# Kernel optimization log

Measured on AMD Instinct MI355X. Metric: run time of the kernel, lower is better.

## Reference

```python
import jax, jax.numpy as jnp
import numpy as np

N = 50000      # nodes per graph side
E = 800000     # edges per graph side
G = 128        # number of graphs in the batch
D = 256        # input feature dim
L = 1024       # number of output labels
NEG_SLOPE = 0.2


def _gat_layer(x, src, dst, W, a_src, a_dst, b, n_nodes):
    """Single-head GATConv with self-loops already included in (src, dst)."""
    h = x @ W                                   # [N, F]
    s_src = h @ a_src                           # [N] per-node source score
    s_dst = h @ a_dst                           # [N] per-node dest score
    e = jax.nn.leaky_relu(s_src[src] + s_dst[dst], NEG_SLOPE)   # [E']
    m = jax.ops.segment_max(e, dst, num_segments=n_nodes)        # segment softmax (stable)
    ex = jnp.exp(e - m[dst])
    denom = jax.ops.segment_sum(ex, dst, num_segments=n_nodes)
    alpha = ex / denom[dst]                     # [E']
    out = jax.ops.segment_sum(h[src] * alpha[:, None], dst, num_segments=n_nodes)
    return out + b


def _mean_pool(x, batch, n_graphs):
    s = jax.ops.segment_sum(x, batch, num_segments=n_graphs)
    cnt = jax.ops.segment_sum(jnp.ones((x.shape[0],), x.dtype), batch, num_segments=n_graphs)
    return s / jnp.maximum(cnt, 1.0)[:, None]


def setup_inputs() -> dict:
    key = jax.random.key(0)
    ks = jax.random.split(key, 24)
    p = lambda k, shape: (jax.random.normal(k, shape, jnp.float32) * 0.05)
    inp = {
        "x_s": jax.random.normal(ks[0], (N, D), jnp.float32),
        "x_t": jax.random.normal(ks[1], (N, D), jnp.float32),
        "edge_index_s": jax.random.randint(ks[2], (2, E), 0, N, jnp.int32),
        "edge_index_t": jax.random.randint(ks[3], (2, E), 0, N, jnp.int32),
        "xs_batch": jnp.sort(jax.random.randint(ks[4], (N,), 0, G, jnp.int32)),
        "xt_batch": jnp.sort(jax.random.randint(ks[5], (N,), 0, G, jnp.int32)),
        # source-graph GAT layers: 256->128, 128->64
        "Ws1": p(ks[6], (D, D // 2)), "as1_src": p(ks[7], (D // 2,)), "as1_dst": p(ks[8], (D // 2,)), "bs1": jnp.zeros((D // 2,), jnp.float32),
        "Ws2": p(ks[9], (D // 2, D // 4)), "as2_src": p(ks[10], (D // 4,)), "as2_dst": p(ks[11], (D // 4,)), "bs2": jnp.zeros((D // 4,), jnp.float32),
        # target-graph GAT layers
        "Wt1": p(ks[12], (D, D // 2)), "at1_src": p(ks[13], (D // 2,)), "at1_dst": p(ks[14], (D // 2,)), "bt1": jnp.zeros((D // 2,), jnp.float32),
        "Wt2": p(ks[15], (D // 2, D // 4)), "at2_src": p(ks[16], (D // 4,)), "at2_dst": p(ks[17], (D // 4,)), "bt2": jnp.zeros((D // 4,), jnp.float32),
        # classifier head
        "Wlin": p(ks[18], (D // 4, L)), "blin": jnp.zeros((L,), jnp.float32),
    }
    return inp


def reference(x_s, x_t, edge_index_s, edge_index_t, xs_batch, xt_batch,
              Ws1, as1_src, as1_dst, bs1, Ws2, as2_src, as2_dst, bs2,
              Wt1, at1_src, at1_dst, bt1, Wt2, at2_src, at2_dst, bt2,
              Wlin, blin):
    loop = jnp.arange(N, dtype=edge_index_s.dtype)
    src_s = jnp.concatenate([edge_index_s[0], loop])   # add self-loops (PyG default)
    dst_s = jnp.concatenate([edge_index_s[1], loop])
    src_t = jnp.concatenate([edge_index_t[0], loop])
    dst_t = jnp.concatenate([edge_index_t[1], loop])

    x1 = jax.nn.relu(_gat_layer(x_s, src_s, dst_s, Ws1, as1_src, as1_dst, bs1, N))
    x2 = jax.nn.relu(_gat_layer(x1, src_s, dst_s, Ws2, as2_src, as2_dst, bs2, N))
    xs = _mean_pool(x2, xs_batch, G)                   # [G, 64]

    x3 = jax.nn.relu(_gat_layer(x_t, src_t, dst_t, Wt1, at1_src, at1_dst, bt1, N))
    x4 = jax.nn.relu(_gat_layer(x3, src_t, dst_t, Wt2, at2_src, at2_dst, bt2, N))
    xt = _mean_pool(x4, xt_batch, G)                   # [G, 64]

    out = (xs + xt) @ Wlin + blin                      # [G, L]
    return jax.nn.sigmoid(out)
```

## Files before the change

### kernel.cpp

```cpp
#include <hip/hip_runtime.h>
#include <hip/hip_bf16.h>
#include <math.h>

constexpr int Nn   = 50000;
constexpr int Ecnt = 800000;
constexpr int Gn   = 128;
constexpr int Din  = 256;
constexpr int Lout = 1024;

constexpr int BKT_SH = 7;
constexpr int NBKT   = (Nn + 127) >> BKT_SH;
constexpr int CHUNK  = 4096;
constexpr int EBC    = (Ecnt + CHUNK - 1) / CHUNK;
constexpr size_t HS  = (size_t)Nn * 64;

typedef __attribute__((ext_vector_type(8))) short short8;
typedef __attribute__((ext_vector_type(4))) float f32x4;
typedef __attribute__((ext_vector_type(2))) float v2f;

__device__ __forceinline__ float lrelu(float x) { return x >= 0.f ? x : 0.2f * x; }

__device__ __forceinline__ float bflo(uint32_t v) { return __uint_as_float(v << 16); }
__device__ __forceinline__ float bfhi(uint32_t v) { return __uint_as_float(v & 0xffff0000u); }
__device__ __forceinline__ uint32_t f2bf(float f) {
    uint32_t x = __float_as_uint(f);
    return (x + 0x7fffu + ((x >> 16) & 1u)) >> 16;
}
__device__ __forceinline__ uint32_t packbf(float lo, float hi) {
    return f2bf(lo) | (f2bf(hi) << 16);
}

__global__ __launch_bounds__(512) void bkt_scan2(const int* __restrict__ bkt_cnt_b,
                                                 int* __restrict__ bkt_ptr_b,
                                                 int* __restrict__ bkt_cur_b,
                                                 int* __restrict__ row_ptr_b) {
    int side = blockIdx.x;
    const int* bkt_cnt = bkt_cnt_b + (size_t)side * (NBKT + 1);
    int* bkt_ptr = bkt_ptr_b + (size_t)side * (NBKT + 1);
    int* bkt_cur = bkt_cur_b + (size_t)side * (NBKT + 1);
    int* row_ptr = row_ptr_b + (size_t)side * (Nn + 1);
    __shared__ int buf[512];
    int t = threadIdx.x;
    int v = (t < NBKT) ? bkt_cnt[t] : 0;
    buf[t] = v;
    __syncthreads();
    for (int off = 1; off < 512; off <<= 1) {
        int x = (t >= off) ? buf[t - off] : 0;
        __syncthreads();
        buf[t] += x;
        __syncthreads();
    }
    if (t < NBKT) {
        int excl = buf[t] - v;
        bkt_ptr[t] = excl;
        bkt_cur[t] = excl;
    }
    if (t == 511) {
        bkt_ptr[NBKT] = buf[511];
        row_ptr[Nn]   = buf[511];
    }
}

__global__ __launch_bounds__(256) void bkt_scatter2(const int* __restrict__ e0,
                                                    const int* __restrict__ e1,
                                                    int* __restrict__ bkt_cur_b,
                                                    uint32_t* __restrict__ bkt_edges_b, int E) {
    int side = blockIdx.y;
    const int* src = side ? e1 : e0;
    const int* dst = src + E;
    int* bkt_cur = bkt_cur_b + (size_t)side * (NBKT + 1);
    uint32_t* bkt_edges = bkt_edges_b + (size_t)side * Ecnt;
    __shared__ int h[NBKT];
    __shared__ int cur[NBKT];
    for (int i = threadIdx.x; i < NBKT; i += 256) h[i] = 0;
    __syncthreads();
    int base = blockIdx.x * CHUNK;
    int end = min(base + CHUNK, E);
    for (int i = base + threadIdx.x; i < end; i += 256)
        atomicAdd(&h[dst[i] >> BKT_SH], 1);
    __syncthreads();
    for (int i = threadIdx.x; i < NBKT; i += 256) {
        int c = h[i];
        h[i] = c ? atomicAdd(&bkt_cur[i], c) : 0;
        cur[i] = 0;
    }
    __syncthreads();
    for (int i = base + threadIdx.x; i < end; i += 256) {
        int d = dst[i], b = d >> BKT_SH;
        int pos = h[b] + atomicAdd(&cur[b], 1);
        bkt_edges[pos] = (uint32_t)src[i] | ((uint32_t)(d & 127) << 16);
    }
}

__global__ __launch_bounds__(256) void csr_finalize2(const uint32_t* __restrict__ bkt_edges_b,
                                                     const int* __restrict__ bkt_ptr_b,
                                                     int* __restrict__ row_ptr_b,
                                                     int* __restrict__ csr_b, int n) {
    int side = blockIdx.y;
    const uint32_t* bkt_edges = bkt_edges_b + (size_t)side * Ecnt;
    const int* bkt_ptr = bkt_ptr_b + (size_t)side * (NBKT + 1);
    int* row_ptr = row_ptr_b + (size_t)side * (Nn + 1);
    int* csr = csr_b + (size_t)side * Ecnt;
    int b = blockIdx.x;
    int base = bkt_ptr[b];
    int cnt  = bkt_ptr[b + 1] - base;
    __shared__ int hist[128], curs[128], sc[128];
    int t = threadIdx.x;
    if (t < 128) hist[t] = 0;
    __syncthreads();
    for (int i = t; i < cnt; i += 256)
        atomicAdd(&hist[(bkt_edges[base + i] >> 16) & 127], 1);
    __syncthreads();
    if (t < 128) sc[t] = hist[t];
    __syncthreads();
    for (int off = 1; off < 128; off <<= 1) {
        int x = (t >= off && t < 128) ? sc[t - off] : 0;
        __syncthreads();
        if (t < 128) sc[t] += x;
        __syncthreads();
    }
    if (t < 128) {
        int excl = sc[t] - hist[t];
        int node = (b << BKT_SH) + t;
        if (node < n) row_ptr[node] = base + excl;
        curs[t] = excl;
    }
    __syncthreads();
    for (int i = t; i < cnt; i += 256) {
        uint32_t e = bkt_edges[base + i];
        int pos = atomicAdd(&curs[(e >> 16) & 127], 1);
        csr[base + pos] = (int)(e & 0xFFFFu);
    }
}

template<int MF, int NF, int KT, bool BF16A, bool FUSE_COUNT>
__global__ __launch_bounds__(256) void mfma_gemm2(
        const void* __restrict__ A0, const void* __restrict__ A1,
        const float* __restrict__ B0, const float* __restrict__ B1,
        uint32_t* __restrict__ Cb, size_t cstride,
        const float* __restrict__ as0, const float* __restrict__ as1,
        const float* __restrict__ ad0, const float* __restrict__ ad1,
        float* __restrict__ ssrc_b, float* __restrict__ sdst_b,
        int M,
        const int* __restrict__ e0, const int* __restrict__ e1,
        int* __restrict__ bkt_cnt_b) {
    constexpr int BM  = 4 * MF * 16;
    constexpr int BN  = NF * 16;
    constexpr int KD  = KT / 2;
    constexpr int LDB = KD + 4;
    constexpr int S   = KT / 32;
    constexpr int BSH = (BN == 128) ? 7 : 6;
    __shared__ uint32_t Bl[BN][LDB];
    int side = blockIdx.y;

    if constexpr (FUSE_COUNT) {
        int gb = (M + BM - 1) / BM;
        if ((int)blockIdx.x >= gb) {
            int chunk = blockIdx.x - gb;
            const int* dst = (side ? e1 : e0) + Ecnt;
            int* bkt_cnt = bkt_cnt_b + (size_t)side * (NBKT + 1);
            int* hh = (int*)&Bl[0][0];
            for (int i = threadIdx.x; i < NBKT; i += 256) hh[i] = 0;
            __syncthreads();
            int base = chunk * CHUNK;
            int end = min(base + CHUNK, Ecnt);
            for (int i = base + threadIdx.x; i < end; i += 256)
                atomicAdd(&hh[dst[i] >> BKT_SH], 1);
            __syncthreads();
            for (int i = threadIdx.x; i < NBKT; i += 256) {
                int c = hh[i];
                if (c) atomicAdd(&bkt_cnt[i], c);
            }
            return;
        }
    }

    const void* Av = side ? A1 : A0;
    const float* B = side ? B1 : B0;
    const float* Asrc = side ? as1 : as0;
    const float* Adst = side ? ad1 : ad0;
    uint32_t* C = Cb + (size_t)side * cstride;
    float* ssrc = ssrc_b + (size_t)side * Nn;
    float* sdst = sdst_b + (size_t)side * Nn;

    int tid  = threadIdx.x;
    int lane = tid & 63;
    int wid  = tid >> 6;
    int bm = blockIdx.x * BM;

    for (int idx = tid; idx < BN * KD; idx += 256) {
        int n  = idx & (BN - 1);
        int kd = idx >> BSH;
        float b0 = B[(size_t)(2 * kd) * BN + n];
        float b1 = B[(size_t)(2 * kd + 1) * BN + n];
        Bl[n][kd] = packbf(b0, b1);
    }
    __syncthreads();

    int lr = lane & 15, lk = lane >> 4;
    int wrow = bm + wid * (MF * 16);

    const float*    ArF[MF];
    const uint32_t* ArU[MF];
    #pragma unroll
    for (int mf = 0; mf < MF; mf++) {
        int r = wrow + mf * 16 + lr;
        r = r < M ? r : (M - 1);
        if constexpr (BF16A) ArU[mf] = (const uint32_t*)Av + (size_t)r * KD;
        else                 ArF[mf] = (const float*)Av + (size_t)r * KT;
    }

    f32x4 acc[MF][NF];
    #pragma unroll
    for (int i = 0; i < MF; i++)
        #pragma unroll
        for (int j = 0; j < NF; j++) acc[i][j] = (f32x4){0.f, 0.f, 0.f, 0.f};

    uint4  ru[2][MF];
    float4 rf0[2][MF], rf1[2][MF];

    auto LOADRAW = [&](int ks, int b) {
        #pragma unroll
        for (int mf = 0; mf < MF; mf++) {
            if constexpr (BF16A) {
                ru[b][mf] = *(const uint4*)(ArU[mf] + ks * 16 + lk * 4);
            } else {
                const float* p = ArF[mf] + ks * 32 + lk * 8;
                rf0[b][mf] = *(const float4*)p;
                rf1[b][mf] = *(const float4*)(p + 4);
            }
        }
    };

    LOADRAW(0, 0);
    #pragma unroll
    for (int ks = 0; ks < S; ks++) {
        if (ks + 1 < S) LOADRAW(ks + 1, (ks + 1) & 1);
        short8 af[MF];
        #pragma unroll
        for (int mf = 0; mf < MF; mf++) {
            if constexpr (BF16A) {
                af[mf] = __builtin_bit_cast(short8, ru[ks & 1][mf]);
            } else {
                float4 f0 = rf0[ks & 1][mf], f1 = rf1[ks & 1][mf];
                uint4 t;
                t.x = packbf(f0.x, f0.y);
                t.y = packbf(f0.z, f0.w);
                t.z = packbf(f1.x, f1.y);
                t.w = packbf(f1.z, f1.w);
                af[mf] = __builtin_bit_cast(short8, t);
            }
        }
        short8 bf[NF];
        #pragma unroll
        for (int nf = 0; nf < NF; nf++)
            bf[nf] = *(const short8*)&Bl[nf * 16 + lr][ks * 16 + lk * 4];
        #pragma unroll
        for (int mf = 0; mf < MF; mf++)
            #pragma unroll
            for (int nf = 0; nf < NF; nf++)
                acc[mf][nf] = __builtin_amdgcn_mfma_f32_16x16x32_bf16(af[mf], bf[nf], acc[mf][nf], 0, 0, 0);
    }

    int lg = lane >> 4;
    {
        float a_s[NF], a_d[NF];
        #pragma unroll
        for (int nf = 0; nf < NF; nf++) {
            a_s[nf] = Asrc[nf * 16 + lr];
            a_d[nf] = Adst[nf * 16 + lr];
        }
        #pragma unroll
        for (int mf = 0; mf < MF; mf++) {
            #pragma unroll
            for (int j = 0; j < 4; j++) {
                float ps = 0.f, pd = 0.f;
                #pragma unroll
                for (int nf = 0; nf < NF; nf++) {
                    float v = acc[mf][nf][j];
                    ps += v * a_s[nf];
                    pd += v * a_d[nf];
                }
                #pragma unroll
                for (int o = 1; o < 16; o <<= 1) {
                    ps += __shfl_xor(ps, o);
                    pd += __shfl_xor(pd, o);
                }
                int row = wrow + mf * 16 + lg * 4 + j;
                if (lr == 0 && row < M) {
                    ssrc[row] = ps;
                    sdst[row] = pd;
                }
            }
        }
    }
    #pragma unroll
    for (int mf = 0; mf < MF; mf++) {
        #pragma unroll
        for (int nf = 0; nf < NF; nf++) {
            int col = nf * 16 + lr;
            #pragma unroll
            for (int j = 0; j < 4; j++) {
                int row = wrow + mf * 16 + lg * 4 + j;
                float v = acc[mf][nf][j];
                float w1 = __shfl_xor(v, 1);
                uint32_t p01 = (uint32_t)__builtin_amdgcn_cvt_pk_fp8_f32(v, w1, 0, false);
                uint32_t p23 = __shfl_xor(p01, 2);
                if (((lane & 3) == 0) && row < M)
                    C[(size_t)row * (BN >> 2) + (col >> 2)] = (p01 & 0xffffu) | (p23 << 16);
            }
        }
    }
}

template<int F>
__global__ __launch_bounds__(256) void attn_agg2(const uint32_t* __restrict__ hb,
        const float* __restrict__ ssrc_b, const float* __restrict__ sdst_b,
        const int* __restrict__ row_ptr_b, const int* __restrict__ csr_b,
        const float* __restrict__ bias0, const float* __restrict__ bias1,
        uint32_t* __restrict__ xout_b, int n) {
    constexpr size_t HSTR = (size_t)Nn * (F / 4);
    constexpr int HD = F / 4;
    constexpr int XD = F / 2;
    int side = blockIdx.y;
    const uint32_t* h = hb + (size_t)side * HSTR;
    const float* ssrc = ssrc_b + (size_t)side * Nn;
    const float* sdst = sdst_b + (size_t)side * Nn;
    const int* row_ptr = row_ptr_b + (size_t)side * (Nn + 1);
    const int* csr_src = csr_b + (size_t)side * Ecnt;
    const float* bias = side ? bias1 : bias0;
    uint32_t* xout = xout_b + (size_t)side * HS;

    int wave = (blockIdx.x * blockDim.x + threadIdx.x) >> 6;
    int lane = threadIdx.x & 63;
    int half = lane >> 5;
    int lane5 = lane & 31;
    int wid = wave * 2 + half;
    if (wid >= n) return;
    int beg = row_ptr[wid], end = row_ptr[wid + 1];
    int deg = end - beg;
    float sd = sdst[wid];
    float eself = lrelu(ssrc[wid] + sd);
    int base32 = lane & 32;

    v2f a0 = {0.f, 0.f}, a1 = {0.f, 0.f}, a2 = {0.f, 0.f}, a3 = {0.f, 0.f};
    auto FMA8 = [&](uint2 u, float wj) {
        v2f p0 = __builtin_amdgcn_cvt_pk_f32_fp8(u.x, false);
        v2f p1 = __builtin_amdgcn_cvt_pk_f32_fp8(u.x, true);
        v2f p2 = __builtin_amdgcn_cvt_pk_f32_fp8(u.y, false);
        v2f p3 = __builtin_amdgcn_cvt_pk_f32_fp8(u.y, true);
        v2f wv = {wj, wj};
        a0 += p0 * wv; a1 += p1 * wv; a2 += p2 * wv; a3 += p3 * wv;
    };

    if (deg <= 32) {
        int p = beg + lane5;
        bool act = lane5 < deg;
        int s = act ? csr_src[p] : 0;
        float e = act ? lrelu(ssrc[s] + sd) : -1e30f;
        float m = fmaxf(eself, e);
        #pragma unroll
        for (int o = 16; o; o >>= 1) m = fmaxf(m, __shfl_xor(m, o));
        float ex = act ? __expf(e - m) : 0.f;
        float dsum = ex;
        #pragma unroll
        for (int o = 16; o; o >>= 1) dsum += __shfl_xor(dsum, o);
        float exself = __expf(eself - m);
        dsum += exself;
        float inv = 1.f / dsum;
        float w = ex * inv;
        float wself = exself * inv;

        if constexpr (F == 128) {
            int slot = (lane >> 4) & 1, i = lane & 15;
            size_t foff = 2 * i;
            if (slot == 0) FMA8(*(const uint2*)(h + (size_t)wid * HD + foff), wself);
            int j = slot;
            for (; j + 6 < deg; j += 8) {
                float w0 = __shfl(w, base32 | j),       w1 = __shfl(w, base32 | (j + 2));
                float w2 = __shfl(w, base32 | (j + 4)), w3 = __shfl(w, base32 | (j + 6));
                int   s0 = __shfl(s, base32 | j),       s1 = __shfl(s, base32 | (j + 2));
                int   s2 = __shfl(s, base32 | (j + 4)), s3 = __shfl(s, base32 | (j + 6));
                uint2 u0 = *(const uint2*)(h + (size_t)s0 * HD + foff);
                uint2 u1 = *(const uint2*)(h + (size_t)s1 * HD + foff);
                uint2 u2 = *(const uint2*)(h + (size_t)s2 * HD + foff);
                uint2 u3 = *(const uint2*)(h + (size_t)s3 * HD + foff);
                FMA8(u0, w0); FMA8(u1, w1); FMA8(u2, w2); FMA8(u3, w3);
            }
            for (; j < deg; j += 2) {
                float w0 = __shfl(w, base32 | j);
                int   s0 = __shfl(s, base32 | j);
                FMA8(*(const uint2*)(h + (size_t)s0 * HD + foff), w0);
            }
            a0[0] += __shfl_xor(a0[0], 16); a0[1] += __shfl_xor(a0[1], 16);
            a1[0] += __shfl_xor(a1[0], 16); a1[1] += __shfl_xor(a1[1], 16);
            a2[0] += __shfl_xor(a2[0], 16); a2[1] += __shfl_xor(a2[1], 16);
            a3[0] += __shfl_xor(a3[0], 16); a3[1] += __shfl_xor(a3[1], 16);
            if (!(lane & 16)) {
                float r0 = fmaxf(a0[0] + bias[8*i],   0.f), r1 = fmaxf(a0[1] + bias[8*i+1], 0.f);
                float r2 = fmaxf(a1[0] + bias[8*i+2], 0.f), r3 = fmaxf(a1[1] + bias[8*i+3], 0.f);
                float r4 = fmaxf(a2[0] + bias[8*i+4], 0.f), r5 = fmaxf(a2[1] + bias[8*i+5], 0.f);
                float r6 = fmaxf(a3[0] + bias[8*i+6], 0.f), r7 = fmaxf(a3[1] + bias[8*i+7], 0.f);
                *(uint4*)(xout + (size_t)wid * XD + 4 * i) =
                    make_uint4(packbf(r0, r1), packbf(r2, r3), packbf(r4, r5), packbf(r6, r7));
            }
        } else {
            int g = (lane >> 3) & 3, i = lane & 7;
            size_t foff = 2 * i;
            if (g == 0) FMA8(*(const uint2*)(h + (size_t)wid * HD + foff), wself);
            int j = g;
            for (; j + 12 < deg; j += 16) {
                float w0 = __shfl(w, base32 | j),       w1 = __shfl(w, base32 | (j + 4));
                float w2 = __shfl(w, base32 | (j + 8)), w3 = __shfl(w, base32 | (j + 12));
                int   s0 = __shfl(s, base32 | j),       s1 = __shfl(s, base32 | (j + 4));
                int   s2 = __shfl(s, base32 | (j + 8)), s3 = __shfl(s, base32 | (j + 12));
                uint2 u0 = *(const uint2*)(h + (size_t)s0 * HD + foff);
                uint2 u1 = *(const uint2*)(h + (size_t)s1 * HD + foff);
                uint2 u2 = *(const uint2*)(h + (size_t)s2 * HD + foff);
                uint2 u3 = *(const uint2*)(h + (size_t)s3 * HD + foff);
                FMA8(u0, w0); FMA8(u1, w1); FMA8(u2, w2); FMA8(u3, w3);
            }
            for (; j < deg; j += 4) {
                float w0 = __shfl(w, base32 | j);
                int   s0 = __shfl(s, base32 | j);
                FMA8(*(const uint2*)(h + (size_t)s0 * HD + foff), w0);
            }
            #pragma unroll
            for (int o = 8; o <= 16; o <<= 1) {
                a0[0] += __shfl_xor(a0[0], o); a0[1] += __shfl_xor(a0[1], o);
                a1[0] += __shfl_xor(a1[0], o); a1[1] += __shfl_xor(a1[1], o);
                a2[0] += __shfl_xor(a2[0], o); a2[1] += __shfl_xor(a2[1], o);
                a3[0] += __shfl_xor(a3[0], o); a3[1] += __shfl_xor(a3[1], o);
            }
            if (!(lane & 24)) {
                float r0 = fmaxf(a0[0] + bias[8*i],   0.f), r1 = fmaxf(a0[1] + bias[8*i+1], 0.f);
                float r2 = fmaxf(a1[0] + bias[8*i+2], 0.f), r3 = fmaxf(a1[1] + bias[8*i+3], 0.f);
                float r4 = fmaxf(a2[0] + bias[8*i+4], 0.f), r5 = fmaxf(a2[1] + bias[8*i+5], 0.f);
                float r6 = fmaxf(a3[0] + bias[8*i+6], 0.f), r7 = fmaxf(a3[1] + bias[8*i+7], 0.f);
                *(uint4*)(xout + (size_t)wid * XD + 4 * i) =
                    make_uint4(packbf(r0, r1), packbf(r2, r3), packbf(r4, r5), packbf(r6, r7));
            }
        }
        return;
    }

    float m = eself;
    for (int p = beg + lane5; p < end; p += 32)
        m = fmaxf(m, lrelu(ssrc[csr_src[p]] + sd));
    #pragma unroll
    for (int o = 16; o; o >>= 1) m = fmaxf(m, __shfl_xor(m, o));
    float dsum = (lane5 == 0) ? __expf(eself - m) : 0.f;
    for (int p = beg + lane5; p < end; p += 32)
        dsum += __expf(lrelu(ssrc[csr_src[p]] + sd) - m);
    #pragma unroll
    for (int o = 16; o; o >>= 1) dsum += __shfl_xor(dsum, o);
    float inv = 1.f / dsum;
    float wself = __expf(eself - m) * inv;

    if constexpr (F == 128) {
        int slot = (lane >> 4) & 1, i = lane & 15;
        size_t foff = 2 * i;
        if (slot == 0) FMA8(*(const uint2*)(h + (size_t)wid * HD + foff), wself);
        for (int j = slot; j < deg; j += 2) {
            int sj = csr_src[beg + j];
            float wj = __expf(lrelu(ssrc[sj] + sd) - m) * inv;
            FMA8(*(const uint2*)(h + (size_t)sj * HD + foff), wj);
        }
        a0[0] += __shfl_xor(a0[0], 16); a0[1] += __shfl_xor(a0[1], 16);
        a1[0] += __shfl_xor(a1[0], 16); a1[1] += __shfl_xor(a1[1], 16);
        a2[0] += __shfl_xor(a2[0], 16); a2[1] += __shfl_xor(a2[1], 16);
        a3[0] += __shfl_xor(a3[0], 16); a3[1] += __shfl_xor(a3[1], 16);
        if (!(lane & 16)) {
            float r0 = fmaxf(a0[0] + bias[8*i],   0.f), r1 = fmaxf(a0[1] + bias[8*i+1], 0.f);
            float r2 = fmaxf(a1[0] + bias[8*i+2], 0.f), r3 = fmaxf(a1[1] + bias[8*i+3], 0.f);
            float r4 = fmaxf(a2[0] + bias[8*i+4], 0.f), r5 = fmaxf(a2[1] + bias[8*i+5], 0.f);
            float r6 = fmaxf(a3[0] + bias[8*i+6], 0.f), r7 = fmaxf(a3[1] + bias[8*i+7], 0.f);
            *(uint4*)(xout + (size_t)wid * XD + 4 * i) =
                make_uint4(packbf(r0, r1), packbf(r2, r3), packbf(r4, r5), packbf(r6, r7));
        }
    } else {
        int g = (lane >> 3) & 3, i = lane & 7;
        size_t foff = 2 * i;
        if (g == 0) FMA8(*(const uint2*)(h + (size_t)wid * HD + foff), wself);
        for (int j = g; j < deg; j += 4) {
            int sj = csr_src[beg + j];
            float wj = __expf(lrelu(ssrc[sj] + sd) - m) * inv;
            FMA8(*(const uint2*)(h + (size_t)sj * HD + foff), wj);
        }
        #pragma unroll
        for (int o = 8; o <= 16; o <<= 1) {
            a0[0] += __shfl_xor(a0[0], o); a0[1] += __shfl_xor(a0[1], o);
            a1[0] += __shfl_xor(a1[0], o); a1[1] += __shfl_xor(a1[1], o);
            a2[0] += __shfl_xor(a2[0], o); a2[1] += __shfl_xor(a2[1], o);
            a3[0] += __shfl_xor(a3[0], o); a3[1] += __shfl_xor(a3[1], o);
        }
        if (!(lane & 24)) {
            float r0 = fmaxf(a0[0] + bias[8*i],   0.f), r1 = fmaxf(a0[1] + bias[8*i+1], 0.f);
            float r2 = fmaxf(a1[0] + bias[8*i+2], 0.f), r3 = fmaxf(a1[1] + bias[8*i+3], 0.f);
            float r4 = fmaxf(a2[0] + bias[8*i+4], 0.f), r5 = fmaxf(a2[1] + bias[8*i+5], 0.f);
            float r6 = fmaxf(a3[0] + bias[8*i+6], 0.f), r7 = fmaxf(a3[1] + bias[8*i+7], 0.f);
            *(uint4*)(xout + (size_t)wid * XD + 4 * i) =
                make_uint4(packbf(r0, r1), packbf(r2, r3), packbf(r4, r5), packbf(r6, r7));
        }
    }
}

__global__ __launch_bounds__(256) void pool2(const uint32_t* __restrict__ xb,
                                             const int* __restrict__ bat0,
                                             const int* __restrict__ bat1,
                                             float* __restrict__ pooled_b, int n) {
    int side = blockIdx.y;
    const uint32_t* x = xb + (size_t)side * HS;
    const int* batch = side ? bat1 : bat0;
    float* pooled = pooled_b + (size_t)side * Gn * 64;
    int g = blockIdx.x;
    int tid = threadIdx.x;
    __shared__ int s_lo, s_hi;
    if (tid == 0) {
        int lo = 0, hi = n;
        while (lo < hi) { int mid = (lo + hi) >> 1; if (batch[mid] < g) lo = mid + 1; else hi = mid; }
        s_lo = lo;
        int lo2 = lo, hi2 = n;
        while (lo2 < hi2) { int mid = (lo2 + hi2) >> 1; if (batch[mid] < g + 1) lo2 = mid + 1; else hi2 = mid; }
        s_hi = lo2;
    }
    __syncthreads();
    int lo = s_lo, hi = s_hi;
    int grp = tid >> 5, col = tid & 31;
    float a0 = 0.f, a1 = 0.f;
    for (int i = lo + grp; i < hi; i += 8) {
        uint32_t v = x[(size_t)i * 32 + col];
        a0 += bflo(v);
        a1 += bfhi(v);
    }
    __shared__ float red0[8][32], red1[8][32];
    red0[grp][col] = a0;
    red1[grp][col] = a1;
    __syncthreads();
    if (tid < 32) {
        float s0 = 0.f, s1 = 0.f;
        #pragma unroll
        for (int r = 0; r < 8; r++) { s0 += red0[r][tid]; s1 += red1[r][tid]; }
        float c = fmaxf((float)(hi - lo), 1.f);
        pooled[g * 64 + 2 * tid]     = s0 / c;
        pooled[g * 64 + 2 * tid + 1] = s1 / c;
    }
}

__global__ __launch_bounds__(256) void head_kernel(const float* __restrict__ xs,
                                                   const float* __restrict__ xt,
                                                   const float* __restrict__ Wlin,
                                                   const float* __restrict__ blin,
                                                   float* __restrict__ out) {
    int g = blockIdx.y;
    int c = blockIdx.x * 256 + threadIdx.x;
    __shared__ float z[64];
    if (threadIdx.x < 64) z[threadIdx.x] = xs[g * 64 + threadIdx.x] + xt[g * 64 + threadIdx.x];
    __syncthreads();
    float a0 = 0.f, a1 = 0.f, a2 = 0.f, a3 = 0.f;
    #pragma unroll
    for (int k = 0; k < 64; k += 4) {
        a0 += z[k]     * Wlin[(size_t)(k)     * Lout + c];
        a1 += z[k + 1] * Wlin[(size_t)(k + 1) * Lout + c];
        a2 += z[k + 2] * Wlin[(size_t)(k + 2) * Lout + c];
        a3 += z[k + 3] * Wlin[(size_t)(k + 3) * Lout + c];
    }
    float acc = (a0 + a1) + (a2 + a3) + blin[c];
    out[(size_t)g * Lout + c] = 1.f / (1.f + expf(-acc));
}

extern "C" void kernel_launch(void* const* d_in, const int* in_sizes, int n_in,
                              void* d_out, int out_size, void* d_ws, size_t ws_size,
                              hipStream_t stream) {
    size_t off = 0;
    auto alloc = [&](size_t bytes) -> void* {
        void* p = (char*)d_ws + off;
        off += (bytes + 255) & ~(size_t)255;
        return p;
    };
    uint32_t* hbuf    = (uint32_t*)alloc(2 * (size_t)Nn * 32 * 4);
    uint32_t* xbuf    = (uint32_t*)alloc(2 * HS * 4);
    float* ssrc       = (float*)alloc(2 * (size_t)Nn * 4);
    float* sdst       = (float*)alloc(2 * (size_t)Nn * 4);
    int*   row_ptr    = (int*)alloc(2 * (size_t)(Nn + 1) * 4);
    int*   csr        = (int*)alloc(2 * (size_t)Ecnt * 4);
    uint32_t* bkt_edges = (uint32_t*)alloc(2 * (size_t)Ecnt * 4);
    int*   bkt_cnt    = (int*)alloc(2 * (size_t)(NBKT + 1) * 4);
    int*   bkt_ptr    = (int*)alloc(2 * (size_t)(NBKT + 1) * 4);
    int*   bkt_cur    = (int*)alloc(2 * (size_t)(NBKT + 1) * 4);
    float* pooled     = (float*)alloc(2 * (size_t)Gn * 64 * 4);

    const int NW2 = (((Nn + 1) / 2) * 64 + 255) / 256;
    const int GB  = (Nn + 127) / 128;

    const float* x_s = (const float*)d_in[0];
    const float* x_t = (const float*)d_in[1];
    const int* ei_s  = (const int*)d_in[2];
    const int* ei_t  = (const int*)d_in[3];
    const int* bat_s = (const int*)d_in[4];
    const int* bat_t = (const int*)d_in[5];
    const float *Ws1 = (const float*)d_in[6],  *as1s = (const float*)d_in[7],
                *as1d = (const float*)d_in[8],  *bs1 = (const float*)d_in[9];
    const float *Ws2 = (const float*)d_in[10], *as2s = (const float*)d_in[11],
                *as2d = (const float*)d_in[12], *bs2 = (const float*)d_in[13];
    const float *Wt1 = (const float*)d_in[14], *at1s = (const float*)d_in[15],
                *at1d = (const float*)d_in[16], *bt1 = (const float*)d_in[17];
    const float *Wt2 = (const float*)d_in[18], *at2s = (const float*)d_in[19],
                *at2d = (const float*)d_in[20], *bt2 = (const float*)d_in[21];
    const float *Wlin = (const float*)d_in[22], *blin = (const float*)d_in[23];

    hipMemsetAsync(bkt_cnt, 0, 2 * (size_t)(NBKT + 1) * 4, stream);
    mfma_gemm2<2, 8, 256, false, true><<<dim3(GB + EBC, 2), 256, 0, stream>>>(
        x_s, x_t, Ws1, Wt1, hbuf, (size_t)Nn * 32, as1s, at1s, as1d, at1d, ssrc, sdst, Nn,
        ei_s, ei_t, bkt_cnt);
    bkt_scan2<<<2, 512, 0, stream>>>(bkt_cnt, bkt_ptr, bkt_cur, row_ptr);
    bkt_scatter2<<<dim3(EBC, 2), 256, 0, stream>>>(ei_s, ei_t, bkt_cur, bkt_edges, Ecnt);
    csr_finalize2<<<dim3(NBKT, 2), 256, 0, stream>>>(bkt_edges, bkt_ptr, row_ptr, csr, Nn);
    attn_agg2<128><<<dim3(NW2, 2), 256, 0, stream>>>(hbuf, ssrc, sdst, row_ptr, csr, bs1, bt1, xbuf, Nn);
    mfma_gemm2<2, 4, 128, true, false><<<dim3(GB, 2), 256, 0, stream>>>(
        xbuf, xbuf + HS, Ws2, Wt2, hbuf, (size_t)Nn * 16, as2s, at2s, as2d, at2d, ssrc, sdst, Nn,
        nullptr, nullptr, nullptr);
    attn_agg2<64><<<dim3(NW2, 2), 256, 0, stream>>>(hbuf, ssrc, sdst, row_ptr, csr, bs2, bt2, xbuf, Nn);
    pool2<<<dim3(Gn, 2), 256, 0, stream>>>(xbuf, bat_s, bat_t, pooled, Nn);
    head_kernel<<<dim3(Lout / 256, Gn), 256, 0, stream>>>(pooled, pooled + (size_t)Gn * 64,
                                                          Wlin, blin, (float*)d_out);
}
```

Baseline: 211.5 us.

## Shrink GEMM block to 64 rows and stage B weights in K-halves

The MFMA GEMM now uses one 16-row fragment per wave (64-row blocks instead of 128) and loads the bf16 weight tile into shared memory in halves of at most 128 K, with a barrier between halves. This cuts per-block LDS and register use to raise occupancy and doubles the block count for better CU fill. The cost is more blocks that each re-stage the full weight matrix, extra syncs, and less reuse of each B fragment across rows.

```diff
diff --git a/kernel.cpp b/kernel.cpp
--- a/kernel.cpp
+++ b/kernel.cpp
@@ -133,7 +133,7 @@
     }
 }
 
-template<int MF, int NF, int KT, bool BF16A, bool FUSE_COUNT>
+template<int NF, int KT, bool BF16A, bool FUSE_COUNT>
 __global__ __launch_bounds__(256) void mfma_gemm2(
         const void* __restrict__ A0, const void* __restrict__ A1,
         const float* __restrict__ B0, const float* __restrict__ B1,
@@ -144,12 +144,15 @@
         int M,
         const int* __restrict__ e0, const int* __restrict__ e1,
         int* __restrict__ bkt_cnt_b) {
-    constexpr int BM  = 4 * MF * 16;
-    constexpr int BN  = NF * 16;
-    constexpr int KD  = KT / 2;
-    constexpr int LDB = KD + 4;
-    constexpr int S   = KT / 32;
-    constexpr int BSH = (BN == 128) ? 7 : 6;
+    constexpr int BM   = 64;
+    constexpr int BN   = NF * 16;
+    constexpr int KH   = (KT > 128) ? 128 : KT;
+    constexpr int HALVES = KT / KH;
+    constexpr int HD2  = KH / 2;
+    constexpr int LDB  = HD2 + 4;
+    constexpr int S2   = KH / 32;
+    constexpr int S    = KT / 32;
+    constexpr int BSH  = (BN == 128) ? 7 : 6;
     __shared__ uint32_t Bl[BN][LDB];
     int side = blockIdx.y;
 
@@ -187,79 +190,68 @@
     int lane = tid & 63;
     int wid  = tid >> 6;
     int bm = blockIdx.x * BM;
-
-    for (int idx = tid; idx < BN * KD; idx += 256) {
-        int n  = idx & (BN - 1);
-        int kd = idx >> BSH;
-        float b0 = B[(size_t)(2 * kd) * BN + n];
-        float b1 = B[(size_t)(2 * kd + 1) * BN + n];
-        Bl[n][kd] = packbf(b0, b1);
-    }
-    __syncthreads();
-
     int lr = lane & 15, lk = lane >> 4;
-    int wrow = bm + wid * (MF * 16);
-
-    const float*    ArF[MF];
-    const uint32_t* ArU[MF];
+    int wrow = bm + wid * 16;
+
+    int arow = wrow + lr;
+    arow = arow < M ? arow : (M - 1);
+    const float*    ArF = nullptr;
+    const uint32_t* ArU = nullptr;
+    if constexpr (BF16A) ArU = (const uint32_t*)Av + (size_t)arow * (KT / 2);
+    else                 ArF = (const float*)Av + (size_t)arow * KT;
+
+    f32x4 acc[NF];
     #pragma unroll
-    for (int mf = 0; mf < MF; mf++) {
-        int r = wrow + mf * 16 + lr;
-        r = r < M ? r : (M - 1);
-        if constexpr (BF16A) ArU[mf] = (const uint32_t*)Av + (size_t)r * KD;
-        else                 ArF[mf] = (const float*)Av + (size_t)r * KT;
-    }
-
-    f32x4 acc[MF][NF];
-    #pragma unroll
-    for (int i = 0; i < MF; i++)
-        #pragma unroll
-        for (int j = 0; j < NF; j++) acc[i][j] = (f32x4){0.f, 0.f, 0.f, 0.f};
-
-    uint4  ru[2][MF];
-    float4 rf0[2][MF], rf1[2][MF];
-
-    auto LOADRAW = [&](int ks, int b) {
-        #pragma unroll
-        for (int mf = 0; mf < MF; mf++) {
-            if constexpr (BF16A) {
-                ru[b][mf] = *(const uint4*)(ArU[mf] + ks * 16 + lk * 4);
-            } else {
-                const float* p = ArF[mf] + ks * 32 + lk * 8;
-                rf0[b][mf] = *(const float4*)p;
-                rf1[b][mf] = *(const float4*)(p + 4);
-            }
+    for (int j = 0; j < NF; j++) acc[j] = (f32x4){0.f, 0.f, 0.f, 0.f};
+
+    uint4  ru[2];
+    float4 rf0[2], rf1[2];
+    auto LOADRAW = [&](int gks, int b) {
+        if constexpr (BF16A) {
+            ru[b] = *(const uint4*)(ArU + gks * 16 + lk * 4);
+        } else {
+            const float* p = ArF + gks * 32 + lk * 8;
+            rf0[b] = *(const float4*)p;
+            rf1[b] = *(const float4*)(p + 4);
         }
     };
 
     LOADRAW(0, 0);
     #pragma unroll
-    for (int ks = 0; ks < S; ks++) {
-        if (ks + 1 < S) LOADRAW(ks + 1, (ks + 1) & 1);
-        short8 af[MF];
-        #pragma unroll
-        for (int mf = 0; mf < MF; mf++) {
+    for (int h = 0; h < HALVES; h++) {
+        if (h > 0) __syncthreads();
+        for (int idx = tid; idx < BN * HD2; idx += 256) {
+            int n  = idx & (BN - 1);
+            int kd = idx >> BSH;
+            float b0 = B[(size_t)(h * KH + 2 * kd) * BN + n];
+            float b1 = B[(size_t)(h * KH + 2 * kd + 1) * BN + n];
+            Bl[n][kd] = packbf(b0, b1);
+        }
+        __syncthreads();
+        #pragma unroll
+        for (int ks = 0; ks < S2; ks++) {
+            int gks = h * S2 + ks;
+            if (gks + 1 < S) LOADRAW(gks + 1, (gks + 1) & 1);
+            short8 af;
             if constexpr (BF16A) {
-                af[mf] = __builtin_bit_cast(short8, ru[ks & 1][mf]);
+                af = __builtin_bit_cast(short8, ru[gks & 1]);
             } else {
-                float4 f0 = rf0[ks & 1][mf], f1 = rf1[ks & 1][mf];
+                float4 f0 = rf0[gks & 1], f1 = rf1[gks & 1];
                 uint4 t;
                 t.x = packbf(f0.x, f0.y);
                 t.y = packbf(f0.z, f0.w);
                 t.z = packbf(f1.x, f1.y);
                 t.w = packbf(f1.z, f1.w);
-                af[mf] = __builtin_bit_cast(short8, t);
-            }
-        }
-        short8 bf[NF];
-        #pragma unroll
-        for (int nf = 0; nf < NF; nf++)
-            bf[nf] = *(const short8*)&Bl[nf * 16 + lr][ks * 16 + lk * 4];
-        #pragma unroll
-        for (int mf = 0; mf < MF; mf++)
+                af = __builtin_bit_cast(short8, t);
+            }
+            short8 bf[NF];
             #pragma unroll
             for (int nf = 0; nf < NF; nf++)
-                acc[mf][nf] = __builtin_amdgcn_mfma_f32_16x16x32_bf16(af[mf], bf[nf], acc[mf][nf], 0, 0, 0);
+                bf[nf] = *(const short8*)&Bl[nf * 16 + lr][ks * 16 + lk * 4];
+            #pragma unroll
+            for (int nf = 0; nf < NF; nf++)
+                acc[nf] = __builtin_amdgcn_mfma_f32_16x16x32_bf16(af, bf[nf], acc[nf], 0, 0, 0);
+        }
     }
 
     int lg = lane >> 4;
@@ -271,44 +263,38 @@
             a_d[nf] = Adst[nf * 16 + lr];
         }
         #pragma unroll
-        for (int mf = 0; mf < MF; mf++) {
+        for (int j = 0; j < 4; j++) {
+            float ps = 0.f, pd = 0.f;
             #pragma unroll
-            for (int j = 0; j < 4; j++) {
-                float ps = 0.f, pd = 0.f;
-                #pragma unroll
-                for (int nf = 0; nf < NF; nf++) {
-                    float v = acc[mf][nf][j];
-                    ps += v * a_s[nf];
-                    pd += v * a_d[nf];
-                }
-                #pragma unroll
-                for (int o = 1; o < 16; o <<= 1) {
-                    ps += __shfl_xor(ps, o);
-                    pd += __shfl_xor(pd, o);
-                }
-                int row = wrow + mf * 16 + lg * 4 + j;
-                if (lr == 0 && row < M) {
-                    ssrc[row] = ps;
-                    sdst[row] = pd;
-                }
+            for (int nf = 0; nf < NF; nf++) {
+                float v = acc[nf][j];
+                ps += v * a_s[nf];
+                pd += v * a_d[nf];
+            }
+            #pragma unroll
+            for (int o = 1; o < 16; o <<= 1) {
+                ps += __shfl_xor(ps, o);
+                pd += __shfl_xor(pd, o);
+            }
+            int row = wrow + lg * 4 + j;
+            if (lr == 0 && row < M) {
+                ssrc[row] = ps;
+                sdst[row] = pd;
             }
         }
     }
     #pragma unroll
-    for (int mf = 0; mf < MF; mf++) {
-        #pragma unroll
-        for (int nf = 0; nf < NF; nf++) {
-            int col = nf * 16 + lr;
-            #pragma unroll
-            for (int j = 0; j < 4; j++) {
-                int row = wrow + mf * 16 + lg * 4 + j;
-                float v = acc[mf][nf][j];
-                float w1 = __shfl_xor(v, 1);
-                uint32_t p01 = (uint32_t)__builtin_amdgcn_cvt_pk_fp8_f32(v, w1, 0, false);
-                uint32_t p23 = __shfl_xor(p01, 2);
-                if (((lane & 3) == 0) && row < M)
-                    C[(size_t)row * (BN >> 2) + (col >> 2)] = (p01 & 0xffffu) | (p23 << 16);
-            }
+    for (int nf = 0; nf < NF; nf++) {
+        int col = nf * 16 + lr;
+        #pragma unroll
+        for (int j = 0; j < 4; j++) {
+            int row = wrow + lg * 4 + j;
+            float v = acc[nf][j];
+            float w1 = __shfl_xor(v, 1);
+            uint32_t p01 = (uint32_t)__builtin_amdgcn_cvt_pk_fp8_f32(v, w1, 0, false);
+            uint32_t p23 = __shfl_xor(p01, 2);
+            if (((lane & 3) == 0) && row < M)
+                C[(size_t)row * (BN >> 2) + (col >> 2)] = (p01 & 0xffffu) | (p23 << 16);
         }
     }
 }
@@ -591,7 +577,7 @@
     float* pooled     = (float*)alloc(2 * (size_t)Gn * 64 * 4);
 
     const int NW2 = (((Nn + 1) / 2) * 64 + 255) / 256;
-    const int GB  = (Nn + 127) / 128;
+    const int GB  = (Nn + 63) / 64;
 
     const float* x_s = (const float*)d_in[0];
     const float* x_t = (const float*)d_in[1];
@@ -610,14 +596,14 @@
     const float *Wlin = (const float*)d_in[22], *blin = (const float*)d_in[23];
 
     hipMemsetAsync(bkt_cnt, 0, 2 * (size_t)(NBKT + 1) * 4, stream);
-    mfma_gemm2<2, 8, 256, false, true><<<dim3(GB + EBC, 2), 256, 0, stream>>>(
+    mfma_gemm2<8, 256, false, true><<<dim3(GB + EBC, 2), 256, 0, stream>>>(
         x_s, x_t, Ws1, Wt1, hbuf, (size_t)Nn * 32, as1s, at1s, as1d, at1d, ssrc, sdst, Nn,
         ei_s, ei_t, bkt_cnt);
     bkt_scan2<<<2, 512, 0, stream>>>(bkt_cnt, bkt_ptr, bkt_cur, row_ptr);
     bkt_scatter2<<<dim3(EBC, 2), 256, 0, stream>>>(ei_s, ei_t, bkt_cur, bkt_edges, Ecnt);
     csr_finalize2<<<dim3(NBKT, 2), 256, 0, stream>>>(bkt_edges, bkt_ptr, row_ptr, csr, Nn);
     attn_agg2<128><<<dim3(NW2, 2), 256, 0, stream>>>(hbuf, ssrc, sdst, row_ptr, csr, bs1, bt1, xbuf, Nn);
-    mfma_gemm2<2, 4, 128, true, false><<<dim3(GB, 2), 256, 0, stream>>>(
+    mfma_gemm2<4, 128, true, false><<<dim3(GB, 2), 256, 0, stream>>>(
         xbuf, xbuf + HS, Ws2, Wt2, hbuf, (size_t)Nn * 16, as2s, at2s, as2d, at2d, ssrc, sdst, Nn,
         nullptr, nullptr, nullptr);
     attn_agg2<64><<<dim3(NW2, 2), 256, 0, stream>>>(hbuf, ssrc, sdst, row_ptr, csr, bs2, bt2, xbuf, Nn);
```

Result: faster. 206.0 us (-2.6%).
